# Performance work log

Measured on AMD Instinct MI355X. Metric: run time of the kernel, lower is better.

## Reference

```python
import jax, jax.numpy as jnp
import numpy as np

B, S, D = 1, 2048, 2048
H, KV, HD = 16, 4, 128
E, TOPK, F = 8, 2, 2048
THETA = 500000.0
CLIP = 8.0
EPS = 1e-5


def setup_inputs() -> dict:
    key = jax.random.key(0)
    ks = jax.random.split(key, 8)
    sc = 0.02
    return {
        "hidden_states": jax.random.normal(ks[0], (B, S, D), jnp.float32),
        "position_ids": jnp.arange(S, dtype=jnp.int64)[None, :].repeat(B, axis=0),
        "ln1_w": jnp.ones((D,), jnp.float32),
        "ln2_w": jnp.ones((D,), jnp.float32),
        "wqkv": jax.random.normal(ks[1], (D, (H + 2 * KV) * HD), jnp.float32) * sc,
        "wo": jax.random.normal(ks[2], (H * HD, D), jnp.float32) * sc,
        "router_w": jax.random.normal(ks[3], (E, D), jnp.float32) * sc,
        "w1": jax.random.normal(ks[4], (E, D, F), jnp.float32) * sc,
        "v1": jax.random.normal(ks[5], (E, D, F), jnp.float32) * sc,
        "w2": jax.random.normal(ks[6], (E, F, D), jnp.float32) * sc,
    }


def _layernorm(x, w):
    mu = jnp.mean(x, axis=-1, keepdims=True)
    var = jnp.mean((x - mu) ** 2, axis=-1, keepdims=True)
    return (x - mu) * jax.lax.rsqrt(var + EPS) * w


def _rotate_half(x):
    x1, x2 = jnp.split(x, 2, axis=-1)
    return jnp.concatenate([-x2, x1], axis=-1)


def _rope(pos):
    inv_freq = 1.0 / (THETA ** (jnp.arange(0, HD, 2, dtype=jnp.float32) / HD))
    ang = pos.astype(jnp.float32)[..., None] * inv_freq  # [B,S,HD/2]
    ang = jnp.concatenate([ang, ang], axis=-1)  # [B,S,HD]
    return jnp.cos(ang)[:, None], jnp.sin(ang)[:, None]  # [B,1,S,HD]


def _forward(hidden_states, position_ids, ln1_w, ln2_w, wqkv, wo, router_w, w1, v1, w2):
    x = hidden_states
    # --- attention sublayer ---
    h = _layernorm(x, ln1_w)
    qkv = jnp.clip(h @ wqkv, -CLIP, CLIP)  # [B,S,(H+2KV)*HD]
    q, k, v = jnp.split(qkv, [H * HD, (H + KV) * HD], axis=-1)
    q = q.reshape(B, S, H, HD).transpose(0, 2, 1, 3)   # [B,H,S,HD]
    k = k.reshape(B, S, KV, HD).transpose(0, 2, 1, 3)  # [B,KV,S,HD]
    v = v.reshape(B, S, KV, HD).transpose(0, 2, 1, 3)
    cos, sin = _rope(position_ids)
    q = q * cos + _rotate_half(q) * sin
    k = k * cos + _rotate_half(k) * sin
    rep = H // KV
    k = jnp.repeat(k, rep, axis=1)  # [B,H,S,HD]
    v = jnp.repeat(v, rep, axis=1)
    scores = jnp.einsum("bhqd,bhkd->bhqk", q, k) / np.sqrt(HD).astype(np.float32)
    causal = jnp.tril(jnp.ones((S, S), bool))
    scores = jnp.where(causal, scores, jnp.finfo(scores.dtype).min)
    probs = jax.nn.softmax(scores, axis=-1)
    attn = jnp.einsum("bhqk,bhkd->bhqd", probs, v)
    attn = attn.transpose(0, 2, 1, 3).reshape(B, S, H * HD) @ wo
    x = x + attn
    # --- MoE FFN sublayer ---
    h = _layernorm(x, ln2_w).reshape(B * S, D)  # [T,D]
    logits = h @ router_w.T                      # [T,E]
    rp = jax.nn.softmax(logits, axis=-1)
    top_w, top_i = jax.lax.top_k(rp, TOPK)       # [T,K]
    top_w = top_w / jnp.sum(top_w, axis=-1, keepdims=True)
    T = B * S
    gate = jnp.zeros((T, E), h.dtype).at[jnp.arange(T)[:, None], top_i].add(top_w)
    g = jax.nn.silu(jnp.einsum("td,edf->tef", h, w1)) * jnp.einsum("td,edf->tef", h, v1)
    y = jnp.einsum("tef,efd,te->td", g, w2, gate)
    x = x + y.reshape(B, S, D)
    return x


def reference(hidden_states, position_ids, ln1_w, ln2_w, wqkv, wo, router_w, w1, v1, w2):
    return _forward(hidden_states, position_ids, ln1_w, ln2_w, wqkv, wo, router_w, w1, v1, w2)
```

## Files before the change

kernel.cpp:

```cpp
#include <hip/hip_runtime.h>

#define S_LEN 2048
#define DMODEL 2048
#define NH 16
#define NKV 4
#define HD 128
#define NE 8
#define FF 2048
#define QKV_N 3072

typedef __attribute__((ext_vector_type(8))) short short8;
typedef __attribute__((ext_vector_type(4))) float f32x4;

__device__ inline unsigned short f2bf(float f) {
  unsigned int u = __builtin_bit_cast(unsigned int, f);
  u += 0x7fffu + ((u >> 16) & 1u);
  return (unsigned short)(u >> 16);
}
__device__ inline float bf2f(unsigned short h) {
  unsigned int u = ((unsigned int)h) << 16;
  return __builtin_bit_cast(float, u);
}
__device__ inline void split2(float v, unsigned short& h, unsigned short& l) {
  h = f2bf(v);
  l = f2bf(v - bf2f(h));
}


__device__ inline void gload16(const void* g, void* l) {
  __builtin_amdgcn_global_load_lds((const __attribute__((address_space(1))) unsigned int*)g,
                                   (__attribute__((address_space(3))) unsigned int*)l,
                                   16, 0, 0);
}
__device__ inline void stageB_chunk(const unsigned short* __restrict__ chunk,
                                    unsigned short* __restrict__ lds) {
  int w = threadIdx.x >> 6, l = threadIdx.x & 63;
  const unsigned short* s = chunk + w * 1024 + l * 8;
  unsigned short* d = lds + w * 1024;
  gload16(s, d);
  gload16(s + 512, d + 512);
}

#define WVM0   asm volatile("s_waitcnt vmcnt(0)" ::: "memory")
#define WVM4   asm volatile("s_waitcnt vmcnt(4)" ::: "memory")
#define WVM6   asm volatile("s_waitcnt vmcnt(6)" ::: "memory")
#define WVM8   asm volatile("s_waitcnt vmcnt(8)" ::: "memory")
#define WVM12  asm volatile("s_waitcnt vmcnt(12)" ::: "memory")
#define WAIT_ALL  asm volatile("s_waitcnt vmcnt(0) lgkmcnt(0)" ::: "memory")
#define WAIT_LDS  asm volatile("s_waitcnt lgkmcnt(0)" ::: "memory")
#define SCHEDBAR  __builtin_amdgcn_sched_barrier(0)
#define BAR       __builtin_amdgcn_s_barrier()


__device__ inline void mma16(const unsigned short* As, const unsigned short* Bs,
                             int wr, int wc, f32x4 acc[4][4]) {
  int l = threadIdx.x & 63;
  int lr = l & 15, lg = l >> 4;
  int qoff = ((lg ^ ((lr ^ (lr >> 2)) & 3)) << 3);
  short8 a[4], b[4];
#pragma unroll
  for (int m = 0; m < 4; m++)
    a[m] = *(const short8*)(As + (wr + m * 16 + lr) * 32 + qoff);
#pragma unroll
  for (int n = 0; n < 4; n++)
    b[n] = *(const short8*)(Bs + (wc + n * 16 + lr) * 32 + qoff);
#pragma unroll
  for (int m = 0; m < 4; m++)
#pragma unroll
    for (int n = 0; n < 4; n++)
      acc[m][n] = __builtin_amdgcn_mfma_f32_16x16x32_bf16(a[m], b[n], acc[m][n], 0, 0, 0);
}

__device__ inline void mma16_dualB(const unsigned short* As, const unsigned short* Bs1,
                                   const unsigned short* Bs2, int wr, int wc,
                                   f32x4 acc1[4][4], f32x4 acc2[4][4]) {
  int l = threadIdx.x & 63;
  int lr = l & 15, lg = l >> 4;
  int qoff = ((lg ^ ((lr ^ (lr >> 2)) & 3)) << 3);
  short8 a[4], b1[4], b2[4];
#pragma unroll
  for (int m = 0; m < 4; m++)
    a[m] = *(const short8*)(As + (wr + m * 16 + lr) * 32 + qoff);
#pragma unroll
  for (int n = 0; n < 4; n++) {
    b1[n] = *(const short8*)(Bs1 + (wc + n * 16 + lr) * 32 + qoff);
    b2[n] = *(const short8*)(Bs2 + (wc + n * 16 + lr) * 32 + qoff);
  }
#pragma unroll
  for (int m = 0; m < 4; m++)
#pragma unroll
    for (int n = 0; n < 4; n++) {
      acc1[m][n] = __builtin_amdgcn_mfma_f32_16x16x32_bf16(a[m], b1[n], acc1[m][n], 0, 0, 0);
      acc2[m][n] = __builtin_amdgcn_mfma_f32_16x16x32_bf16(a[m], b2[n], acc2[m][n], 0, 0, 0);
    }
}

__device__ inline void mma16_split_reg(const unsigned short* Ash, const unsigned short* Asl,
                                       const unsigned short* Bsh, const unsigned short* Bsl,
                                       int wr, int wc, f32x4 acc[4][4]) {
  int l = threadIdx.x & 63;
  int lr = l & 15, lg = l >> 4;
  int qoff = ((lg ^ ((lr ^ (lr >> 2)) & 3)) << 3);
  short8 ah[4], al[4], bh[4], bl[4];
#pragma unroll
  for (int m = 0; m < 4; m++) {
    ah[m] = *(const short8*)(Ash + (wr + m * 16 + lr) * 32 + qoff);
    al[m] = *(const short8*)(Asl + (wr + m * 16 + lr) * 32 + qoff);
  }
#pragma unroll
  for (int n = 0; n < 4; n++) {
    bh[n] = *(const short8*)(Bsh + (wc + n * 16 + lr) * 32 + qoff);
    bl[n] = *(const short8*)(Bsl + (wc + n * 16 + lr) * 32 + qoff);
  }
#pragma unroll
  for (int m = 0; m < 4; m++)
#pragma unroll
    for (int n = 0; n < 4; n++) {
      acc[m][n] = __builtin_amdgcn_mfma_f32_16x16x32_bf16(ah[m], bh[n], acc[m][n], 0, 0, 0);
      acc[m][n] = __builtin_amdgcn_mfma_f32_16x16x32_bf16(ah[m], bl[n], acc[m][n], 0, 0, 0);
      acc[m][n] = __builtin_amdgcn_mfma_f32_16x16x32_bf16(al[m], bh[n], acc[m][n], 0, 0, 0);
    }
}


__global__ __launch_bounds__(256) void k_pack1(const float* __restrict__ src, long ld,
                                               long zs, int nc,
                                               unsigned short* __restrict__ dst) {
  __shared__ float tile[32][132];
  const float* Sp = src + (long)blockIdx.z * zs;
  int c = blockIdx.x, t = threadIdx.x;
  for (int i = 0; i < 4; i++) {
    int kt = blockIdx.y * 4 + i;
    long k0 = (long)kt * 32, n0 = (long)c * 128;
    {
      int k = t >> 3, nn = (t & 7) * 16;
      const float4* p = (const float4*)(Sp + (k0 + k) * ld + n0 + nn);
#pragma unroll
      for (int j = 0; j < 4; j++) *(float4*)&tile[k][nn + j * 4] = p[j];
    }
    __syncthreads();
    size_t cbase = ((size_t)(blockIdx.z * nc + c) * 64 + kt) * 4096;
#pragma unroll
    for (int uu = 0; uu < 2; uu++) {
      int u = t * 2 + uu;
      int n = u >> 2, qp = u & 3;
      int q = qp ^ ((n ^ (n >> 2)) & 3);
      unsigned short hb[8] __attribute__((aligned(16)));
#pragma unroll
      for (int j = 0; j < 8; j++) hb[j] = f2bf(tile[8 * q + j][n]);
      *(uint4*)(dst + cbase + u * 8) = *(const uint4*)hb;
    }
    __syncthreads();
  }
}

__global__ __launch_bounds__(256) void k_pack2(const float* __restrict__ src, long ld,
                                               long zs, int nc,
                                               unsigned short* __restrict__ dh,
                                               unsigned short* __restrict__ dl) {
  __shared__ float tile[32][132];
  const float* Sp = src + (long)blockIdx.z * zs;
  int c = blockIdx.x, t = threadIdx.x;
  for (int i = 0; i < 4; i++) {
    int kt = blockIdx.y * 4 + i;
    long k0 = (long)kt * 32, n0 = (long)c * 128;
    {
      int k = t >> 3, nn = (t & 7) * 16;
      const float4* p = (const float4*)(Sp + (k0 + k) * ld + n0 + nn);
#pragma unroll
      for (int j = 0; j < 4; j++) *(float4*)&tile[k][nn + j * 4] = p[j];
    }
    __syncthreads();
    size_t cbase = ((size_t)(blockIdx.z * nc + c) * 64 + kt) * 4096;
#pragma unroll
    for (int uu = 0; uu < 2; uu++) {
      int u = t * 2 + uu;
      int n = u >> 2, qp = u & 3;
      int q = qp ^ ((n ^ (n >> 2)) & 3);
      unsigned short hb[8] __attribute__((aligned(16)));
      unsigned short lb[8] __attribute__((aligned(16)));
#pragma unroll
      for (int j = 0; j < 8; j++) split2(tile[8 * q + j][n], hb[j], lb[j]);
      *(uint4*)(dh + cbase + u * 8) = *(const uint4*)hb;
      *(uint4*)(dl + cbase + u * 8) = *(const uint4*)lb;
    }
    __syncthreads();
  }
}

__global__ __launch_bounds__(256) void k_packbf(const unsigned short* __restrict__ src,
                                                unsigned short* __restrict__ dst) {
  int ttile = blockIdx.x;
  int z = blockIdx.y;
  const unsigned short* Sp = src + ((size_t)z * S_LEN + (size_t)ttile * 128) * HD;
  size_t ob = ((size_t)z * 64 + (size_t)ttile * 4) * 4096;
  int t = threadIdx.x;
#pragma unroll
  for (int kst = 0; kst < 4; kst++) {
#pragma unroll
    for (int uu = 0; uu < 2; uu++) {
      int u = t * 2 + uu;
      int n = u >> 2, qp = u & 3;
      int q = qp ^ ((n ^ (n >> 2)) & 3);
      *(uint4*)(dst + ob + (size_t)kst * 4096 + u * 8) =
          *(const uint4*)(Sp + (size_t)n * HD + kst * 32 + q * 8);
    }
  }
}

__global__ __launch_bounds__(256) void k_gpack(const unsigned short* __restrict__ h2b,
                                               const int* __restrict__ ptok,
                                               const int* __restrict__ meta,
                                               unsigned short* __restrict__ hAP) {
  int ty = blockIdx.x;
  if (ty >= meta[25]) return;
  int tt = meta[26 + ty];
  int e = tt & 7, m0 = tt >> 3;
  int nvalid = min(128, meta[e] - m0);
  const int* toks = ptok + meta[16 + e] + m0;
  int t = threadIdx.x;
  int r = t >> 2, q = t & 3;
  int s = (r ^ (r >> 2)) & 3;
  for (int kt = blockIdx.y * 8; kt < blockIdx.y * 8 + 8; kt++) {
    unsigned short* dst = hAP + ((size_t)ty * 64 + kt) * 4096;
#pragma unroll
    for (int rr = 0; rr < 2; rr++) {
      int row = r + rr * 64;
      uint4 v = make_uint4(0, 0, 0, 0);
      if (row < nvalid)
        v = *(const uint4*)(h2b + (size_t)toks[row] * DMODEL + kt * 32 + q * 8);
      *(uint4*)(dst + row * 32 + ((q ^ s) << 3)) = v;
    }
  }
}


__global__ __launch_bounds__(256) void k_qkv_s(const unsigned short* __restrict__ APh,
                                               const unsigned short* __restrict__ APl,
                                               const unsigned short* __restrict__ BPh,
                                               const unsigned short* __restrict__ BPl,
                                               float* __restrict__ C) {
  __shared__ unsigned short Ash[2 * 4096], Asl[2 * 4096], Bsh[2 * 4096], Bsl[2 * 4096];
  size_t ab = (size_t)blockIdx.y * 64 * 4096;
  size_t cb = (size_t)blockIdx.x * 64 * 4096;
  int w = threadIdx.x >> 6;
  int wr = (w >> 1) * 64, wc = (w & 1) * 64;
  stageB_chunk(APh + ab, Ash);
  stageB_chunk(APl + ab, Asl);
  stageB_chunk(BPh + cb, Bsh);
  stageB_chunk(BPl + cb, Bsl);
  WAIT_ALL;
  BAR;
  f32x4 acc[4][4] = {};
  for (int kt = 0; kt < 64; kt++) {
    int cur = (kt & 1) << 12, nxt = 4096 - cur;
    if (kt + 1 < 64) {
      size_t o = (size_t)(kt + 1) * 4096;
      stageB_chunk(APh + ab + o, Ash + nxt);
      stageB_chunk(APl + ab + o, Asl + nxt);
      stageB_chunk(BPh + cb + o, Bsh + nxt);
      stageB_chunk(BPl + cb + o, Bsl + nxt);
    }
    SCHEDBAR;
    mma16_split_reg(Ash + cur, Asl + cur, Bsh + cur, Bsl + cur, wr, wc, acc);
    SCHEDBAR;
    WAIT_ALL;
    BAR;
  }
  int row0 = blockIdx.y * 128, col0 = blockIdx.x * 128;
  int l = threadIdx.x & 63;
  int er = wr + ((l >> 4) << 2), ec = wc + (l & 15);
#pragma unroll
  for (int m = 0; m < 4; m++)
#pragma unroll
    for (int n = 0; n < 4; n++)
#pragma unroll
      for (int r = 0; r < 4; r++) {
        float v = acc[m][n][r];
        v = fminf(fmaxf(v, -8.f), 8.f);
        C[(size_t)(row0 + er + m * 16 + r) * QKV_N + col0 + ec + n * 16] = v;
      }
}

__global__ __launch_bounds__(256) void k_wo_s(const unsigned short* __restrict__ APh,
                                              const unsigned short* __restrict__ APl,
                                              const unsigned short* __restrict__ BPh,
                                              const unsigned short* __restrict__ BPl,
                                              const float* __restrict__ resid,
                                              float* __restrict__ x1) {
  __shared__ unsigned short Ash[2 * 4096], Asl[2 * 4096], Bsh[2 * 4096], Bsl[2 * 4096];
  size_t ab = (size_t)blockIdx.y * 64 * 4096;
  size_t cb = (size_t)blockIdx.x * 64 * 4096;
  int w = threadIdx.x >> 6;
  int wr = (w >> 1) * 64, wc = (w & 1) * 64;
  stageB_chunk(APh + ab, Ash);
  stageB_chunk(APl + ab, Asl);
  stageB_chunk(BPh + cb, Bsh);
  stageB_chunk(BPl + cb, Bsl);
  WAIT_ALL;
  BAR;
  f32x4 acc[4][4] = {};
  for (int kt = 0; kt < 64; kt++) {
    int cur = (kt & 1) << 12, nxt = 4096 - cur;
    if (kt + 1 < 64) {
      size_t o = (size_t)(kt + 1) * 4096;
      stageB_chunk(APh + ab + o, Ash + nxt);
      stageB_chunk(APl + ab + o, Asl + nxt);
      stageB_chunk(BPh + cb + o, Bsh + nxt);
      stageB_chunk(BPl + cb + o, Bsl + nxt);
    }
    SCHEDBAR;
    mma16_split_reg(Ash + cur, Asl + cur, Bsh + cur, Bsl + cur, wr, wc, acc);
    SCHEDBAR;
    WAIT_ALL;
    BAR;
  }
  int row0 = blockIdx.y * 128, col0 = blockIdx.x * 128;
  int l = threadIdx.x & 63;
  int er = wr + ((l >> 4) << 2), ec = wc + (l & 15);
#pragma unroll
  for (int m = 0; m < 4; m++)
#pragma unroll
    for (int n = 0; n < 4; n++)
#pragma unroll
      for (int r = 0; r < 4; r++) {
        size_t idx = (size_t)(row0 + er + m * 16 + r) * DMODEL + col0 + ec + n * 16;
        x1[idx] = resid[idx] + acc[m][n][r];
      }
}


__global__ __launch_bounds__(128) void k_flash(const unsigned short* __restrict__ qh,
                                               const unsigned short* __restrict__ ql,
                                               const unsigned short* __restrict__ kPh,
                                               const unsigned short* __restrict__ kPl,
                                               const unsigned short* __restrict__ vPh,
                                               const unsigned short* __restrict__ vPl,
                                               unsigned short* __restrict__ atPh,
                                               unsigned short* __restrict__ atPl) {
  int bid = blockIdx.x;
  int h = (bid & 7) | ((bid >> 8) << 3);
  int rt = (bid >> 3) & 31;
  int kv = h >> 2;
  int ntiles = (rt >> 1) + 1;
  __shared__ float Pds[2][32 * 132];
  int t = threadIdx.x;
  int w = t >> 6, l = t & 63;
  int lr = l & 15, lg = l >> 4;
  int qoff = ((lg ^ ((lr ^ (lr >> 2)) & 3)) << 3);
  int wrow0 = rt * 64 + w * 32;
  const unsigned short* Qbh = qh + (size_t)h * S_LEN * HD;
  const unsigned short* Qbl = ql + (size_t)h * S_LEN * HD;
  const unsigned short* Kch = kPh + (size_t)kv * 64 * 4096;
  const unsigned short* Kcl = kPl + (size_t)kv * 64 * 4096;
  const unsigned short* Vch = vPh + (size_t)kv * 64 * 4096;
  const unsigned short* Vcl = vPl + (size_t)kv * 64 * 4096;
  float* Pw = &Pds[w][0];
  float mrun[2][4], lrun[2][4];
  f32x4 Oc[2][8];
#pragma unroll
  for (int m = 0; m < 2; m++)
#pragma unroll
    for (int r = 0; r < 4; r++) { mrun[m][r] = -3.4e38f; lrun[m][r] = 0.f; }
#pragma unroll
  for (int m = 0; m < 2; m++)
#pragma unroll
    for (int n = 0; n < 8; n++)
#pragma unroll
      for (int r = 0; r < 4; r++) Oc[m][n][r] = 0.f;
  const float scale = 0.08838834764831845f;

  for (int kt = 0; kt < ntiles; kt++) {
    f32x4 Sa[2][8];
#pragma unroll
    for (int m = 0; m < 2; m++)
#pragma unroll
      for (int n = 0; n < 8; n++)
#pragma unroll
        for (int r = 0; r < 4; r++) Sa[m][n][r] = 0.f;
#pragma unroll
    for (int kst = 0; kst < 4; kst++) {
      short8 qfh[2], qfl[2];
#pragma unroll
      for (int m = 0; m < 2; m++) {
        size_t o = (size_t)(wrow0 + m * 16 + lr) * HD + kst * 32 + lg * 8;
        qfh[m] = *(const short8*)(Qbh + o);
        qfl[m] = *(const short8*)(Qbl + o);
      }
      const unsigned short* Kh = Kch + (size_t)(kt * 4 + kst) * 4096;
      const unsigned short* Kl = Kcl + (size_t)(kt * 4 + kst) * 4096;
      short8 bh[8], bl[8];
#pragma unroll
      for (int n = 0; n < 8; n++) {
        bh[n] = *(const short8*)(Kh + (n * 16 + lr) * 32 + qoff);
        bl[n] = *(const short8*)(Kl + (n * 16 + lr) * 32 + qoff);
      }
#pragma unroll
      for (int m = 0; m < 2; m++)
#pragma unroll
        for (int n = 0; n < 8; n++) {
          Sa[m][n] = __builtin_amdgcn_mfma_f32_16x16x32_bf16(qfh[m], bh[n], Sa[m][n], 0, 0, 0);
          Sa[m][n] = __builtin_amdgcn_mfma_f32_16x16x32_bf16(qfh[m], bl[n], Sa[m][n], 0, 0, 0);
          Sa[m][n] = __builtin_amdgcn_mfma_f32_16x16x32_bf16(qfl[m], bh[n], Sa[m][n], 0, 0, 0);
        }
    }
#pragma unroll
    for (int m = 0; m < 2; m++)
#pragma unroll
      for (int r = 0; r < 4; r++) {
        int row = wrow0 + m * 16 + lg * 4 + r;
        float mx = mrun[m][r];
#pragma unroll
        for (int n = 0; n < 8; n++) {
          float v = Sa[m][n][r] * scale;
          int col = kt * 128 + n * 16 + lr;
          v = (col <= row) ? v : -3.4e38f;
          Sa[m][n][r] = v;
          mx = fmaxf(mx, v);
        }
        mx = fmaxf(mx, __shfl_xor(mx, 1));
        mx = fmaxf(mx, __shfl_xor(mx, 2));
        mx = fmaxf(mx, __shfl_xor(mx, 4));
        mx = fmaxf(mx, __shfl_xor(mx, 8));
        float al_ = expf(mrun[m][r] - mx);
        float sum = 0.f;
#pragma unroll
        for (int n = 0; n < 8; n++) {
          float v = Sa[m][n][r];
          float e = (v > -1.0e37f) ? expf(v - mx) : 0.f;
          Sa[m][n][r] = e;
          sum += e;
        }
        sum += __shfl_xor(sum, 1);
        sum += __shfl_xor(sum, 2);
        sum += __shfl_xor(sum, 4);
        sum += __shfl_xor(sum, 8);
        lrun[m][r] = lrun[m][r] * al_ + sum;
        mrun[m][r] = mx;
#pragma unroll
        for (int n = 0; n < 8; n++) Oc[m][n][r] *= al_;
      }
    WAIT_LDS;
    SCHEDBAR;
#pragma unroll
    for (int m = 0; m < 2; m++)
#pragma unroll
      for (int n = 0; n < 8; n++)
#pragma unroll
        for (int r = 0; r < 4; r++)
          Pw[(m * 16 + lg * 4 + r) * 132 + n * 16 + lr] = Sa[m][n][r];
    WAIT_LDS;
    SCHEDBAR;
#pragma unroll
    for (int kst = 0; kst < 4; kst++) {
      const unsigned short* Vh = Vch + (size_t)(kt * 4 + kst) * 4096;
      const unsigned short* Vl = Vcl + (size_t)(kt * 4 + kst) * 4096;
      short8 bh[8], bl[8];
#pragma unroll
      for (int n = 0; n < 8; n++) {
        bh[n] = *(const short8*)(Vh + (n * 16 + lr) * 32 + qoff);
        bl[n] = *(const short8*)(Vl + (n * 16 + lr) * 32 + qoff);
      }
#pragma unroll
      for (int m = 0; m < 2; m++) {
        const float* pp = &Pw[(m * 16 + lr) * 132 + kst * 32 + lg * 8];
        unsigned short ahb[8] __attribute__((aligned(16)));
        unsigned short alb[8] __attribute__((aligned(16)));
#pragma unroll
        for (int j = 0; j < 8; j++) split2(pp[j], ahb[j], alb[j]);
        short8 ah = *(const short8*)ahb;
        short8 al_ = *(const short8*)alb;
#pragma unroll
        for (int n = 0; n < 8; n++) {
          Oc[m][n] = __builtin_amdgcn_mfma_f32_16x16x32_bf16(ah, bh[n], Oc[m][n], 0, 0, 0);
          Oc[m][n] = __builtin_amdgcn_mfma_f32_16x16x32_bf16(ah, bl[n], Oc[m][n], 0, 0, 0);
          Oc[m][n] = __builtin_amdgcn_mfma_f32_16x16x32_bf16(al_, bh[n], Oc[m][n], 0, 0, 0);
        }
      }
    }
  }
#pragma unroll
  for (int m = 0; m < 2; m++)
#pragma unroll
    for (int r = 0; r < 4; r++) {
      int row = wrow0 + m * 16 + lg * 4 + r;
      int rtc = row >> 7, rl = row & 127;
      int sr = (rl ^ (rl >> 2)) & 3;
      float lv = lrun[m][r];
#pragma unroll
      for (int n = 0; n < 8; n++) {
        int col = h * HD + n * 16 + lr;
        size_t off = ((size_t)(rtc * 64 + (col >> 5))) * 4096 + rl * 32 +
                     ((((col & 31) >> 3) ^ sr) << 3) + (col & 7);
        unsigned short hh, ll;
        split2(Oc[m][n][r] / lv, hh, ll);
        atPh[off] = hh;
        atPl[off] = ll;
      }
    }
}


__global__ __launch_bounds__(256) void k_moe1f(const unsigned short* __restrict__ hAP,
                                               const unsigned short* __restrict__ wPa,
                                               const unsigned short* __restrict__ wPb,
                                               const int* __restrict__ meta,
                                               unsigned short* __restrict__ g) {
  int ty = blockIdx.y;
  if (ty >= meta[25]) return;
  int tt = meta[26 + ty];
  int e = tt & 7, m0 = tt >> 3;
  int nvalid = min(128, meta[e] - m0);
  const unsigned short* Ab = hAP + (size_t)ty * 64 * 4096;
  const unsigned short* B1 = wPa + (size_t)(e * 16 + blockIdx.x) * 64 * 4096;
  const unsigned short* B2 = wPb + (size_t)(e * 16 + blockIdx.x) * 64 * 4096;
  __shared__ unsigned short L[3][3][4096];
  int w = threadIdx.x >> 6;
  int wr = (w >> 1) * 64, wc = (w & 1) * 64;
#pragma unroll
  for (int p = 0; p < 3; p++) {
    size_t o = (size_t)p * 4096;
    stageB_chunk(Ab + o, &L[p][0][0]);
    stageB_chunk(B1 + o, &L[p][1][0]);
    stageB_chunk(B2 + o, &L[p][2][0]);
  }
  WVM12;
  BAR;
  f32x4 acc1[4][4] = {}, acc2[4][4] = {};
  int cur = 0;
  for (int kt = 0; kt < 64; kt++) {
    SCHEDBAR;
    mma16_dualB(&L[cur][0][0], &L[cur][1][0], &L[cur][2][0], wr, wc, acc1, acc2);
    SCHEDBAR;
    BAR;
    if (kt + 3 < 64) {
      size_t o = (size_t)(kt + 3) * 4096;
      stageB_chunk(Ab + o, &L[cur][0][0]);
      stageB_chunk(B1 + o, &L[cur][1][0]);
      stageB_chunk(B2 + o, &L[cur][2][0]);
      WVM12;
    } else if (kt + 3 == 64) {
      WVM6;
    } else {
      WVM0;
    }
    BAR;
    cur = (cur == 2) ? 0 : cur + 1;
  }
  int l = threadIdx.x & 63;
  int er = wr + ((l >> 4) << 2), ec = wc + (l & 15);
  int ktf0 = blockIdx.x * 4;
#pragma unroll
  for (int m = 0; m < 4; m++)
#pragma unroll
    for (int n = 0; n < 4; n++)
#pragma unroll
      for (int r = 0; r < 4; r++) {
        int rl = er + m * 16 + r;
        int cc = ec + n * 16;
        float a = acc1[m][n][r];
        float s = a / (1.f + expf(-a));
        unsigned short val = (rl < nvalid) ? f2bf(s * acc2[m][n][r]) : (unsigned short)0;
        int srl = (rl ^ (rl >> 2)) & 3;
        g[((size_t)(ty * 64 + ktf0 + (cc >> 5))) * 4096 + rl * 32 +
          ((((cc & 31) >> 3) ^ srl) << 3) + (cc & 7)] = val;
      }
}

__global__ __launch_bounds__(256) void k_moe2(const unsigned short* __restrict__ gP,
                                              const unsigned short* __restrict__ wP,
                                              const int* __restrict__ ptok,
                                              const float* __restrict__ pw,
                                              const int* __restrict__ meta,
                                              float* __restrict__ out) {
  int ty = blockIdx.y;
  if (ty >= meta[25]) return;
  int tt = meta[26 + ty];
  int e = tt & 7, m0 = tt >> 3;
  int nvalid = min(128, meta[e] - m0);
  long pbase = (long)meta[16 + e] + m0;
  int kc = blockIdx.z;
  const unsigned short* Ab = gP + ((size_t)ty * 64 + kc * 32) * 4096;
  const unsigned short* Bb = wP + ((size_t)(e * 16 + blockIdx.x) * 64 + kc * 32) * 4096;
  __shared__ unsigned short L[3][2][4096];
  int w = threadIdx.x >> 6;
  int wr = (w >> 1) * 64, wc = (w & 1) * 64;
#pragma unroll
  for (int p = 0; p < 3; p++) {
    size_t o = (size_t)p * 4096;
    stageB_chunk(Ab + o, &L[p][0][0]);
    stageB_chunk(Bb + o, &L[p][1][0]);
  }
  WVM8;
  BAR;
  f32x4 acc[4][4] = {};
  int cur = 0;
  for (int kt = 0; kt < 32; kt++) {
    SCHEDBAR;
    mma16(&L[cur][0][0], &L[cur][1][0], wr, wc, acc);
    SCHEDBAR;
    BAR;
    if (kt + 3 < 32) {
      size_t o = (size_t)(kt + 3) * 4096;
      stageB_chunk(Ab + o, &L[cur][0][0]);
      stageB_chunk(Bb + o, &L[cur][1][0]);
      WVM8;
    } else if (kt + 3 == 32) {
      WVM4;
    } else {
      WVM0;
    }
    BAR;
    cur = (cur == 2) ? 0 : cur + 1;
  }
  int col0 = blockIdx.x * 128;
  int l = threadIdx.x & 63;
  int er = wr + ((l >> 4) << 2), ec = wc + (l & 15);
#pragma unroll
  for (int m = 0; m < 4; m++)
#pragma unroll
    for (int n = 0; n < 4; n++)
#pragma unroll
      for (int r = 0; r < 4; r++) {
        int rl = er + m * 16 + r;
        if (rl < nvalid) {
          long p = pbase + rl;
          int tk = ptok[p];
          atomicAdd(&out[(size_t)tk * DMODEL + col0 + ec + n * 16], acc[m][n][r] * pw[p]);
        }
      }
}


__global__ __launch_bounds__(256) void k_ln(const float* __restrict__ x,
                                            const float* __restrict__ w,
                                            unsigned short* __restrict__ obh,
                                            unsigned short* __restrict__ obl,
                                            float* __restrict__ of, int mode) {
  int row = blockIdx.x;
  const float* xr = x + (size_t)row * DMODEL;
  float s = 0.f, ss = 0.f;
  for (int c = threadIdx.x; c < DMODEL; c += 256) {
    float v = xr[c];
    s += v; ss += v * v;
  }
#pragma unroll
  for (int o = 32; o; o >>= 1) { s += __shfl_down(s, o); ss += __shfl_down(ss, o); }
  __shared__ float rs[4], rss[4], mu_s, inv_s;
  int wid = threadIdx.x >> 6;
  if ((threadIdx.x & 63) == 0) { rs[wid] = s; rss[wid] = ss; }
  __syncthreads();
  if (threadIdx.x == 0) {
    float S1 = rs[0] + rs[1] + rs[2] + rs[3];
    float S2 = rss[0] + rss[1] + rss[2] + rss[3];
    float mu = S1 / DMODEL;
    mu_s = mu;
    inv_s = rsqrtf(S2 / DMODEL - mu * mu + 1e-5f);
  }
  __syncthreads();
  float mu = mu_s, inv = inv_s;
  int rt = row >> 7, rl = row & 127;
  int sw = (rl ^ (rl >> 2)) & 3;
  for (int c = threadIdx.x; c < DMODEL; c += 256) {
    float v = (xr[c] - mu) * inv * w[c];
    unsigned short hh, ll;
    split2(v, hh, ll);
    if (mode) {
      size_t off = ((size_t)(rt * 64 + (c >> 5))) * 4096 + rl * 32 +
                   ((((c & 31) >> 3) ^ sw) << 3) + (c & 7);
      obh[off] = hh;
      obl[off] = ll;
    } else {
      obh[(size_t)row * DMODEL + c] = hh;
      obl[(size_t)row * DMODEL + c] = ll;
      of[(size_t)row * DMODEL + c] = v;
    }
  }
}

__global__ void k_rope2(const float* __restrict__ qkv, unsigned short* __restrict__ qh,
                        unsigned short* __restrict__ ql, unsigned short* __restrict__ kh,
                        unsigned short* __restrict__ kl) {
  int t = blockIdx.x;
  int d = threadIdx.x;
  float pf = (float)pow(500000.0, (double)d * (1.0 / 64.0));
  float invf = 1.0f / pf;
  float ang = (float)t * invf;
  float cs = (float)cos((double)ang);
  float sn = (float)sin((double)ang);
  const float* row = qkv + (size_t)t * QKV_N;
  unsigned short hh, ll;
#pragma unroll
  for (int hq = 0; hq < NH; hq++) {
    float a = row[hq * HD + d], b = row[hq * HD + d + 64];
    size_t base = ((size_t)hq * S_LEN + t) * HD;
    split2(a * cs - b * sn, hh, ll); qh[base + d] = hh; ql[base + d] = ll;
    split2(b * cs + a * sn, hh, ll); qh[base + d + 64] = hh; ql[base + d + 64] = ll;
  }
#pragma unroll
  for (int kv = 0; kv < NKV; kv++) {
    float a = row[NH * HD + kv * HD + d], b = row[NH * HD + kv * HD + d + 64];
    size_t base = ((size_t)kv * S_LEN + t) * HD;
    split2(a * cs - b * sn, hh, ll); kh[base + d] = hh; kl[base + d] = ll;
    split2(b * cs + a * sn, hh, ll); kh[base + d + 64] = hh; kl[base + d + 64] = ll;
  }
}

__global__ __launch_bounds__(256) void k_router(const float* __restrict__ h2,
                                                const float* __restrict__ rw,
                                                int* __restrict__ topi,
                                                float* __restrict__ topw,
                                                int* __restrict__ cnt) {
  int t = blockIdx.x;
  __shared__ float hs[DMODEL];
  __shared__ float lg[NE];
  for (int c = threadIdx.x; c < DMODEL; c += 256) hs[c] = h2[(size_t)t * DMODEL + c];
  __syncthreads();
  int grp = threadIdx.x >> 5;
  int ln = threadIdx.x & 31;
  float p = 0.f;
  for (int c = ln; c < DMODEL; c += 32) p += hs[c] * rw[(size_t)grp * DMODEL + c];
#pragma unroll
  for (int o = 16; o; o >>= 1) p += __shfl_down(p, o, 32);
  if (ln == 0) lg[grp] = p;
  __syncthreads();
  if (threadIdx.x == 0) {
    float l0 = -3.4e38f; int i0 = 0;
    for (int e = 0; e < NE; e++)
      if (lg[e] > l0) { l0 = lg[e]; i0 = e; }
    float l1 = -3.4e38f; int i1 = 0;
    for (int e = 0; e < NE; e++)
      if (e != i0 && lg[e] > l1) { l1 = lg[e]; i1 = e; }
    float z = expf(l1 - l0);
    topi[t * 2] = i0; topi[t * 2 + 1] = i1;
    topw[t * 2] = 1.f / (1.f + z); topw[t * 2 + 1] = z / (1.f + z);
    atomicAdd(&cnt[i0], 1);
    atomicAdd(&cnt[i1], 1);
  }
}

__global__ void k_scan(int* __restrict__ meta) {
  if (threadIdx.x == 0 && blockIdx.x == 0) {
    int o = 0, nt = 0;
    for (int e = 0; e < NE; e++) {
      meta[16 + e] = o;
      for (int m0 = 0; m0 < meta[e]; m0 += 128) meta[26 + nt++] = (m0 << 3) | e;
      o += meta[e];
    }
    meta[24] = o;
    meta[25] = nt;
  }
}

__global__ void k_fill(const int* __restrict__ topi, const float* __restrict__ topw,
                       int* __restrict__ meta, int* __restrict__ ptok,
                       float* __restrict__ pw) {
  int t = blockIdx.x * blockDim.x + threadIdx.x;
  if (t >= S_LEN) return;
#pragma unroll
  for (int j = 0; j < 2; j++) {
    int e = topi[t * 2 + j];
    int p = atomicAdd(&meta[8 + e], 1);
    ptok[meta[16 + e] + p] = t;
    pw[meta[16 + e] + p] = topw[t * 2 + j];
  }
}


extern "C" void kernel_launch(void* const* d_in, const int* in_sizes, int n_in,
                              void* d_out, int out_size, void* d_ws, size_t ws_size,
                              hipStream_t stream) {
  (void)in_sizes; (void)n_in; (void)out_size; (void)ws_size;
  const float* x = (const float*)d_in[0];
  const float* ln1w = (const float*)d_in[2];
  const float* ln2w = (const float*)d_in[3];
  const float* wqkv = (const float*)d_in[4];
  const float* wo = (const float*)d_in[5];
  const float* rw = (const float*)d_in[6];
  const float* w1 = (const float*)d_in[7];
  const float* v1 = (const float*)d_in[8];
  const float* w2 = (const float*)d_in[9];
  float* out = (float*)d_out;

  char* wsb = (char*)d_ws;
  const size_t MiB = 1u << 20;
  unsigned short* h1Ph = (unsigned short*)(wsb + 0 * MiB);
  unsigned short* h1Pl = (unsigned short*)(wsb + 8 * MiB);
  float* qkvb = (float*)(wsb + 16 * MiB);
  unsigned short* qh = (unsigned short*)(wsb + 40 * MiB);
  unsigned short* ql = (unsigned short*)(wsb + 48 * MiB);
  unsigned short* kh = (unsigned short*)(wsb + 56 * MiB);
  unsigned short* kl = (unsigned short*)(wsb + 58 * MiB);
  unsigned short* vPh = (unsigned short*)(wsb + 60 * MiB);
  unsigned short* vPl = (unsigned short*)(wsb + 62 * MiB);
  unsigned short* kPh = (unsigned short*)(wsb + 64 * MiB);
  unsigned short* kPl = (unsigned short*)(wsb + 66 * MiB);
  unsigned short* atPh = (unsigned short*)(wsb + 68 * MiB);
  unsigned short* atPl = (unsigned short*)(wsb + 76 * MiB);
  unsigned short* wqkvPh = (unsigned short*)(wsb + 84 * MiB);
  unsigned short* wqkvPl = (unsigned short*)(wsb + 96 * MiB);
  unsigned short* woPh = (unsigned short*)(wsb + 108 * MiB);
  unsigned short* woPl = (unsigned short*)(wsb + 116 * MiB);
  unsigned short* hAP = (unsigned short*)(wsb + 0 * MiB);
  unsigned short* g = (unsigned short*)(wsb + 20 * MiB);
  float* h2f = (float*)(wsb + 40 * MiB);
  unsigned short* h2b = (unsigned short*)(wsb + 56 * MiB);
  unsigned short* h2lo = (unsigned short*)(wsb + 20 * MiB);
  unsigned short* wPa = (unsigned short*)(wsb + 40 * MiB);
  unsigned short* wPb = (unsigned short*)(wsb + 104 * MiB);
  char* small = wsb + 168 * MiB;
  int* topi = (int*)small;
  float* topw = (float*)(small + 16384);
  int* ptok = (int*)(small + 32768);
  float* pw = (float*)(small + 49152);
  int* meta = (int*)(small + 65536);

  k_pack2<<<dim3(QKV_N / 128, 16, 1), 256, 0, stream>>>(wqkv, QKV_N, 0, QKV_N / 128,
                                                        wqkvPh, wqkvPl);
  k_pack2<<<dim3(DMODEL / 128, 16, 1), 256, 0, stream>>>(wo, DMODEL, 0, DMODEL / 128,
                                                         woPh, woPl);

  k_ln<<<S_LEN, 256, 0, stream>>>(x, ln1w, h1Ph, h1Pl, (float*)nullptr, 1);
  k_qkv_s<<<dim3(QKV_N / 128, S_LEN / 128), 256, 0, stream>>>(h1Ph, h1Pl, wqkvPh, wqkvPl,
                                                              qkvb);
  k_rope2<<<S_LEN, 64, 0, stream>>>(qkvb, qh, ql, kh, kl);
  k_pack2<<<dim3(1, 16, NKV), 256, 0, stream>>>(qkvb + (NH + NKV) * HD, QKV_N, HD, 1,
                                                vPh, vPl);
  k_packbf<<<dim3(16, NKV), 256, 0, stream>>>(kh, kPh);
  k_packbf<<<dim3(16, NKV), 256, 0, stream>>>(kl, kPl);
  k_flash<<<512, 128, 0, stream>>>(qh, ql, kPh, kPl, vPh, vPl, atPh, atPl);
  k_wo_s<<<dim3(16, 16), 256, 0, stream>>>(atPh, atPl, woPh, woPl, x, out);

  k_ln<<<S_LEN, 256, 0, stream>>>(out, ln2w, h2b, h2lo, h2f, 0);
  hipMemsetAsync(meta, 0, 512, stream);
  k_router<<<S_LEN, 256, 0, stream>>>(h2f, rw, topi, topw, meta);
  k_scan<<<1, 64, 0, stream>>>(meta);
  k_fill<<<8, 256, 0, stream>>>(topi, topw, meta, ptok, pw);
  k_gpack<<<dim3(40, 8), 256, 0, stream>>>(h2b, ptok, meta, hAP);
  k_pack1<<<dim3(16, 16, NE), 256, 0, stream>>>(w1, FF, (long)DMODEL * FF, 16, wPa);
  k_pack1<<<dim3(16, 16, NE), 256, 0, stream>>>(v1, FF, (long)DMODEL * FF, 16, wPb);
  k_moe1f<<<dim3(16, 40), 256, 0, stream>>>(hAP, wPa, wPb, meta, g);
  k_pack1<<<dim3(16, 16, NE), 256, 0, stream>>>(w2, DMODEL, (long)FF * DMODEL, 16, wPa);
  k_moe2<<<dim3(16, 40, 2), 256, 0, stream>>>(g, wPa, ptok, pw, meta, out);
}
```

Before: 917.6 us.

## Fuse K packing into RoPE and gather MoE tokens directly in moe1

The RoPE kernel now writes rotated K straight into the swizzled packed tile layout, so the two k_packbf launches and their intermediate buffers go away. The MoE first GEMM gathers routed token rows from the bf16 LN output through ptok during its own LDS staging, which removes the separate k_gpack kernel and its packed activation buffer. The gathered loads are scattered rows rather than contiguous chunks, which may lower load efficiency inside the GEMM's pipeline. The workspace layout is also rearranged.

```diff
diff --git a/kernel.cpp b/kernel.cpp
--- a/kernel.cpp
+++ b/kernel.cpp
@@ -185,52 +185,6 @@
       *(uint4*)(dl + cbase + u * 8) = *(const uint4*)lb;
     }
     __syncthreads();
-  }
-}
-
-__global__ __launch_bounds__(256) void k_packbf(const unsigned short* __restrict__ src,
-                                                unsigned short* __restrict__ dst) {
-  int ttile = blockIdx.x;
-  int z = blockIdx.y;
-  const unsigned short* Sp = src + ((size_t)z * S_LEN + (size_t)ttile * 128) * HD;
-  size_t ob = ((size_t)z * 64 + (size_t)ttile * 4) * 4096;
-  int t = threadIdx.x;
-#pragma unroll
-  for (int kst = 0; kst < 4; kst++) {
-#pragma unroll
-    for (int uu = 0; uu < 2; uu++) {
-      int u = t * 2 + uu;
-      int n = u >> 2, qp = u & 3;
-      int q = qp ^ ((n ^ (n >> 2)) & 3);
-      *(uint4*)(dst + ob + (size_t)kst * 4096 + u * 8) =
-          *(const uint4*)(Sp + (size_t)n * HD + kst * 32 + q * 8);
-    }
-  }
-}
-
-__global__ __launch_bounds__(256) void k_gpack(const unsigned short* __restrict__ h2b,
-                                               const int* __restrict__ ptok,
-                                               const int* __restrict__ meta,
-                                               unsigned short* __restrict__ hAP) {
-  int ty = blockIdx.x;
-  if (ty >= meta[25]) return;
-  int tt = meta[26 + ty];
-  int e = tt & 7, m0 = tt >> 3;
-  int nvalid = min(128, meta[e] - m0);
-  const int* toks = ptok + meta[16 + e] + m0;
-  int t = threadIdx.x;
-  int r = t >> 2, q = t & 3;
-  int s = (r ^ (r >> 2)) & 3;
-  for (int kt = blockIdx.y * 8; kt < blockIdx.y * 8 + 8; kt++) {
-    unsigned short* dst = hAP + ((size_t)ty * 64 + kt) * 4096;
-#pragma unroll
-    for (int rr = 0; rr < 2; rr++) {
-      int row = r + rr * 64;
-      uint4 v = make_uint4(0, 0, 0, 0);
-      if (row < nvalid)
-        v = *(const uint4*)(h2b + (size_t)toks[row] * DMODEL + kt * 32 + q * 8);
-      *(uint4*)(dst + row * 32 + ((q ^ s) << 3)) = v;
-    }
   }
 }
 
@@ -501,7 +455,8 @@
 }
 
 
-__global__ __launch_bounds__(256) void k_moe1f(const unsigned short* __restrict__ hAP,
+__global__ __launch_bounds__(256) void k_moe1f(const unsigned short* __restrict__ h2b,
+                                               const int* __restrict__ ptok,
                                                const unsigned short* __restrict__ wPa,
                                                const unsigned short* __restrict__ wPb,
                                                const int* __restrict__ meta,
@@ -511,16 +466,26 @@
   int tt = meta[26 + ty];
   int e = tt & 7, m0 = tt >> 3;
   int nvalid = min(128, meta[e] - m0);
-  const unsigned short* Ab = hAP + (size_t)ty * 64 * 4096;
   const unsigned short* B1 = wPa + (size_t)(e * 16 + blockIdx.x) * 64 * 4096;
   const unsigned short* B2 = wPb + (size_t)(e * 16 + blockIdx.x) * 64 * 4096;
   __shared__ unsigned short L[3][3][4096];
   int w = threadIdx.x >> 6;
+  int lid = threadIdx.x & 63;
   int wr = (w >> 1) * 64, wc = (w & 1) * 64;
+  int r0 = w * 32 + (lid >> 2);
+  int qx = lid & 3;
+  int s0 = (r0 ^ (r0 >> 2)) & 3;
+  long pb = (long)meta[16 + e] + m0;
+  int tk0 = ptok[pb + min(r0, nvalid - 1)];
+  int tk1 = ptok[pb + min(r0 + 16, nvalid - 1)];
+  const unsigned short* a0 = h2b + (size_t)tk0 * DMODEL + ((qx ^ s0) << 3);
+  const unsigned short* a1 = h2b + (size_t)tk1 * DMODEL + ((qx ^ s0) << 3);
 #pragma unroll
   for (int p = 0; p < 3; p++) {
     size_t o = (size_t)p * 4096;
-    stageB_chunk(Ab + o, &L[p][0][0]);
+    unsigned short* dA = &L[p][0][0] + w * 1024;
+    gload16(a0 + p * 32, dA);
+    gload16(a1 + p * 32, dA + 512);
     stageB_chunk(B1 + o, &L[p][1][0]);
     stageB_chunk(B2 + o, &L[p][2][0]);
   }
@@ -535,7 +500,9 @@
     BAR;
     if (kt + 3 < 64) {
       size_t o = (size_t)(kt + 3) * 4096;
-      stageB_chunk(Ab + o, &L[cur][0][0]);
+      unsigned short* dA = &L[cur][0][0] + w * 1024;
+      gload16(a0 + (kt + 3) * 32, dA);
+      gload16(a1 + (kt + 3) * 32, dA + 512);
       stageB_chunk(B1 + o, &L[cur][1][0]);
       stageB_chunk(B2 + o, &L[cur][2][0]);
       WVM12;
@@ -679,8 +646,8 @@
 }
 
 __global__ void k_rope2(const float* __restrict__ qkv, unsigned short* __restrict__ qh,
-                        unsigned short* __restrict__ ql, unsigned short* __restrict__ kh,
-                        unsigned short* __restrict__ kl) {
+                        unsigned short* __restrict__ ql, unsigned short* __restrict__ kPh,
+                        unsigned short* __restrict__ kPl) {
   int t = blockIdx.x;
   int d = threadIdx.x;
   float pf = (float)pow(500000.0, (double)d * (1.0 / 64.0));
@@ -697,12 +664,23 @@
     split2(a * cs - b * sn, hh, ll); qh[base + d] = hh; ql[base + d] = ll;
     split2(b * cs + a * sn, hh, ll); qh[base + d + 64] = hh; ql[base + d + 64] = ll;
   }
+  int tt2 = t >> 7, rl2 = t & 127;
+  int s2 = (rl2 ^ (rl2 >> 2)) & 3;
 #pragma unroll
   for (int kv = 0; kv < NKV; kv++) {
     float a = row[NH * HD + kv * HD + d], b = row[NH * HD + kv * HD + d + 64];
-    size_t base = ((size_t)kv * S_LEN + t) * HD;
-    split2(a * cs - b * sn, hh, ll); kh[base + d] = hh; kl[base + d] = ll;
-    split2(b * cs + a * sn, hh, ll); kh[base + d + 64] = hh; kl[base + d + 64] = ll;
+    float o0 = a * cs - b * sn;
+    float o1 = b * cs + a * sn;
+#pragma unroll
+    for (int half = 0; half < 2; half++) {
+      int col = d + half * 64;
+      float v = half ? o1 : o0;
+      size_t off = ((size_t)(kv * 64 + tt2 * 4 + (col >> 5))) * 4096 + rl2 * 32 +
+                   ((((col & 31) >> 3) ^ s2) << 3) + (col & 7);
+      split2(v, hh, ll);
+      kPh[off] = hh;
+      kPl[off] = ll;
+    }
   }
 }
 
@@ -789,8 +767,6 @@
   float* qkvb = (float*)(wsb + 16 * MiB);
   unsigned short* qh = (unsigned short*)(wsb + 40 * MiB);
   unsigned short* ql = (unsigned short*)(wsb + 48 * MiB);
-  unsigned short* kh = (unsigned short*)(wsb + 56 * MiB);
-  unsigned short* kl = (unsigned short*)(wsb + 58 * MiB);
   unsigned short* vPh = (unsigned short*)(wsb + 60 * MiB);
   unsigned short* vPl = (unsigned short*)(wsb + 62 * MiB);
   unsigned short* kPh = (unsigned short*)(wsb + 64 * MiB);
@@ -801,11 +777,10 @@
   unsigned short* wqkvPl = (unsigned short*)(wsb + 96 * MiB);
   unsigned short* woPh = (unsigned short*)(wsb + 108 * MiB);
   unsigned short* woPl = (unsigned short*)(wsb + 116 * MiB);
-  unsigned short* hAP = (unsigned short*)(wsb + 0 * MiB);
-  unsigned short* g = (unsigned short*)(wsb + 20 * MiB);
+  unsigned short* h2b = (unsigned short*)(wsb + 0 * MiB);
+  unsigned short* h2lo = (unsigned short*)(wsb + 8 * MiB);
+  unsigned short* g = (unsigned short*)(wsb + 16 * MiB);
   float* h2f = (float*)(wsb + 40 * MiB);
-  unsigned short* h2b = (unsigned short*)(wsb + 56 * MiB);
-  unsigned short* h2lo = (unsigned short*)(wsb + 20 * MiB);
   unsigned short* wPa = (unsigned short*)(wsb + 40 * MiB);
   unsigned short* wPb = (unsigned short*)(wsb + 104 * MiB);
   char* small = wsb + 168 * MiB;
@@ -823,11 +798,9 @@
   k_ln<<<S_LEN, 256, 0, stream>>>(x, ln1w, h1Ph, h1Pl, (float*)nullptr, 1);
   k_qkv_s<<<dim3(QKV_N / 128, S_LEN / 128), 256, 0, stream>>>(h1Ph, h1Pl, wqkvPh, wqkvPl,
                                                               qkvb);
-  k_rope2<<<S_LEN, 64, 0, stream>>>(qkvb, qh, ql, kh, kl);
+  k_rope2<<<S_LEN, 64, 0, stream>>>(qkvb, qh, ql, kPh, kPl);
   k_pack2<<<dim3(1, 16, NKV), 256, 0, stream>>>(qkvb + (NH + NKV) * HD, QKV_N, HD, 1,
                                                 vPh, vPl);
-  k_packbf<<<dim3(16, NKV), 256, 0, stream>>>(kh, kPh);
-  k_packbf<<<dim3(16, NKV), 256, 0, stream>>>(kl, kPl);
   k_flash<<<512, 128, 0, stream>>>(qh, ql, kPh, kPl, vPh, vPl, atPh, atPl);
   k_wo_s<<<dim3(16, 16), 256, 0, stream>>>(atPh, atPl, woPh, woPl, x, out);
 
@@ -836,10 +809,9 @@
   k_router<<<S_LEN, 256, 0, stream>>>(h2f, rw, topi, topw, meta);
   k_scan<<<1, 64, 0, stream>>>(meta);
   k_fill<<<8, 256, 0, stream>>>(topi, topw, meta, ptok, pw);
-  k_gpack<<<dim3(40, 8), 256, 0, stream>>>(h2b, ptok, meta, hAP);
   k_pack1<<<dim3(16, 16, NE), 256, 0, stream>>>(w1, FF, (long)DMODEL * FF, 16, wPa);
   k_pack1<<<dim3(16, 16, NE), 256, 0, stream>>>(v1, FF, (long)DMODEL * FF, 16, wPb);
-  k_moe1f<<<dim3(16, 40), 256, 0, stream>>>(hAP, wPa, wPb, meta, g);
+  k_moe1f<<<dim3(16, 40), 256, 0, stream>>>(h2b, ptok, wPa, wPb, meta, g);
   k_pack1<<<dim3(16, 16, NE), 256, 0, stream>>>(w2, DMODEL, (long)FF * DMODEL, 16, wPa);
   k_moe2<<<dim3(16, 40, 2), 256, 0, stream>>>(g, wPa, ptok, pw, meta, out);
 }
```

Result: no change. 912.1 us (-0.6%).
